# Kernel tuning notes

Hardware: AMD Instinct MI355X
Metric: run time of the kernel (lower is better)

The kernel has to match this reference:

```python
import jax, jax.numpy as jnp
import numpy as np

BLOCK_SIZE = 64  # weights per (scale, zero_point) block along in_features


def _dequant(q_weights, q_scales, q_zp):
    # q_weights: [N, K] int codes in [0,16); q_scales/q_zp: [N, K//BLOCK_SIZE]
    N, K = q_weights.shape
    nb = K // BLOCK_SIZE
    q = q_weights.reshape(N, nb, BLOCK_SIZE).astype(q_scales.dtype)
    zp = q_zp.reshape(N, nb, 1).astype(q_scales.dtype)
    s = q_scales.reshape(N, nb, 1)
    return ((q - zp) * s).reshape(N, K)  # [N, K] float


def setup_inputs() -> dict:
    key = jax.random.key(0)
    k1, k2, k3, k4, k5 = jax.random.split(key, 5)
    M, K, N = 4096, 4096, 11008
    nb = K // BLOCK_SIZE
    return {
        "input": jax.random.normal(k1, (M, K), dtype=jnp.float32),
        "q_weights": jax.random.randint(k2, (N, K), 0, 16, dtype=jnp.int32),
        "q_scales": jax.random.uniform(k3, (N, nb), dtype=jnp.float32, minval=0.01, maxval=0.05),
        "q_zp": jax.random.randint(k4, (N, nb), 0, 16, dtype=jnp.int32),
        "bias": jax.random.normal(k5, (N,), dtype=jnp.float32),
    }


def reference(input, q_weights, q_scales, q_zp, bias):
    # Blockwise int4 dequant + GEMM: out[m, n] = sum_k input[m, k] * w[n, k]
    w = _dequant(q_weights, q_scales, q_zp)          # [N, K]
    out = jnp.einsum("mk,nk->mn", input, w)          # [M, N]
    return out + bias[None, :]
```

## Files before the change

kernel.cpp:

```cpp
#include <hip/hip_runtime.h>


#define BM 128
#define BN 128
#define BK 64
#define LDSN 72

typedef __attribute__((ext_vector_type(8))) short bf16x8;
typedef __attribute__((ext_vector_type(4))) float f32x4;

__device__ __forceinline__ unsigned short f2bf(float f) {
    union { float f; unsigned int u; } v; v.f = f;
    unsigned int u = v.u;
    u += 0x7FFFu + ((u >> 16) & 1u);
    return (unsigned short)(u >> 16);
}
__device__ __forceinline__ unsigned int pack2(float a, float b) {
    return (unsigned int)f2bf(a) | ((unsigned int)f2bf(b) << 16);
}

__device__ __forceinline__ void gl_lds16(const void* gp, void* lp) {
    __builtin_amdgcn_global_load_lds(
        (const __attribute__((address_space(1))) unsigned int*)gp,
        (__attribute__((address_space(3))) unsigned int*)lp,
        16, 0, 0);
}

__global__ __launch_bounds__(256)
void a2bf_kernel(const float* __restrict__ A, unsigned short* __restrict__ Ab,
                 long total4)
{
    long t = (long)blockIdx.x * blockDim.x + threadIdx.x;
    if (t >= total4) return;
    float4 v = ((const float4*)A)[t];
    uint2 p; p.x = pack2(v.x, v.y); p.y = pack2(v.z, v.w);
    ((uint2*)Ab)[t] = p;
}

__global__ __launch_bounds__(256)
void dequant_kernel(const int* __restrict__ Q, const float* __restrict__ S,
                    const int* __restrict__ Zp, unsigned short* __restrict__ W,
                    int K, int nb)
{
    const int n = blockIdx.y;
    const int k = (blockIdx.x * 256 + threadIdx.x) * 8;
    if (k >= K) return;
    const int kb = k >> 6;
    const float s  = S[(size_t)n * nb + kb];
    const float zs = (float)Zp[(size_t)n * nb + kb] * s;
    const int4* qp = (const int4*)(Q + (size_t)n * K + k);
    int4 q0 = qp[0], q1 = qp[1];
    uint4 o;
    o.x = pack2((float)q0.x * s - zs, (float)q0.y * s - zs);
    o.y = pack2((float)q0.z * s - zs, (float)q0.w * s - zs);
    o.z = pack2((float)q1.x * s - zs, (float)q1.y * s - zs);
    o.w = pack2((float)q1.z * s - zs, (float)q1.w * s - zs);
    *(uint4*)(W + (size_t)n * K + k) = o;
}


#define G8_BARRIER() do { asm volatile("" ::: "memory");                    \
    __builtin_amdgcn_s_barrier(); asm volatile("" ::: "memory"); } while (0)
#define G8_VMCNT(n) asm volatile("s_waitcnt vmcnt(" #n ")" ::: "memory")
#define G8_LGKM0()  do { asm volatile("s_waitcnt lgkmcnt(0)" ::: "memory"); \
    __builtin_amdgcn_sched_barrier(0); } while (0)

#define G8_STAGE(G, kt, h, base, b)                                          \
  do {                                                                       \
    const unsigned short* _s = (G) + (long)(kt) * 64 + (long)(h) * 128 * K;  \
    gl_lds16(_s + aoff0, (base) + (b) * 32768 + (h) * 16384 + lds0);         \
    gl_lds16(_s + aoff1, (base) + (b) * 32768 + (h) * 16384 + lds1);         \
  } while (0)

#define G8_LOAD_AF(b, mh)                                                    \
  { _Pragma("unroll") for (int _i = 0; _i < 4; ++_i) {                       \
      const int _ra = (mh) * 128 + arow + _i * 16;                           \
      const char* _pa = AsB + (b) * 32768 + _ra * 128;                       \
      af[_i][0] = *(const bf16x8*)(_pa + ck0);                               \
      af[_i][1] = *(const bf16x8*)(_pa + ck1);                               \
  } }

#define G8_LOAD_BF(b, nh)                                                    \
  { _Pragma("unroll") for (int _j = 0; _j < 2; ++_j) {                       \
      const int _rb = (nh) * 128 + brow + _j * 16;                           \
      const char* _pb = BsB + (b) * 32768 + _rb * 128;                       \
      bfg[_j][0] = *(const bf16x8*)(_pb + ck0);                              \
      bfg[_j][1] = *(const bf16x8*)(_pb + ck1);                              \
  } }

#define G8_MFMA(q)                                                           \
  __builtin_amdgcn_s_setprio(1);                                             \
  { _Pragma("unroll") for (int _i = 0; _i < 4; ++_i)                         \
    _Pragma("unroll") for (int _j = 0; _j < 2; ++_j) {                       \
      acc[q][_i][_j] = __builtin_amdgcn_mfma_f32_16x16x32_bf16(              \
          af[_i][0], bfg[_j][0], acc[q][_i][_j], 0, 0, 0);                   \
      acc[q][_i][_j] = __builtin_amdgcn_mfma_f32_16x16x32_bf16(              \
          af[_i][1], bfg[_j][1], acc[q][_i][_j], 0, 0, 0);                   \
  } }                                                                        \
  __builtin_amdgcn_s_setprio(0);

__global__ __launch_bounds__(512, 2)
void gemm8_kernel(const unsigned short* __restrict__ Ab,
                  const unsigned short* __restrict__ Wb,
                  const float* __restrict__ bias, float* __restrict__ C,
                  int M, int N, int K)
{
    __shared__ __align__(16) unsigned short As[2][256][64];
    __shared__ __align__(16) unsigned short Bs[2][256][64];

    const int tid  = threadIdx.x;
    const int m0   = blockIdx.x * 256;
    const int n0   = blockIdx.y * 256;
    const int lane = tid & 63;
    const int wave = tid >> 6;
    const int ww   = wave >> 2;
    const int wv   = wave & 3;
    const int fr   = lane & 15;
    const int quad = lane >> 4;
    const int sw   = fr & 7;

    const int rl0 = tid >> 3;
    const int rl1 = (512 + tid) >> 3;
    const int pp  = tid & 7;
    const long aoff0 = (long)rl0 * K + (long)((pp ^ (rl0 & 7)) * 8);
    const long aoff1 = (long)rl1 * K + (long)((pp ^ (rl1 & 7)) * 8);
    const int lds0 = tid * 16;
    const int lds1 = (512 + tid) * 16;

    const int ck0 = (quad ^ sw) * 16;
    const int ck1 = ((4 + quad) ^ sw) * 16;
    const int arow = ww * 64 + fr;
    const int brow = wv * 32 + fr;

    char* AsB = (char*)&As[0][0][0];
    char* BsB = (char*)&Bs[0][0][0];

    const unsigned short* Ag = Ab + (size_t)m0 * K;
    const unsigned short* Bg = Wb + (size_t)n0 * K;

    f32x4 acc[4][4][2];
    #pragma unroll
    for (int q = 0; q < 4; ++q)
        #pragma unroll
        for (int i = 0; i < 4; ++i)
            #pragma unroll
            for (int j = 0; j < 2; ++j)
                acc[q][i][j] = (f32x4){0.f, 0.f, 0.f, 0.f};

    bf16x8 af[4][2], bfg[2][2];

    G8_STAGE(Ag, 0, 0, AsB, 0);
    G8_STAGE(Bg, 0, 0, BsB, 0);
    G8_STAGE(Ag, 0, 1, AsB, 0);
    G8_STAGE(Bg, 0, 1, BsB, 0);
    G8_STAGE(Ag, 1, 0, AsB, 1);
    G8_STAGE(Bg, 1, 0, BsB, 1);
    G8_VMCNT(4);
    G8_BARRIER();

    const int nit = K / 128;
    for (int it = 0; it < nit - 1; ++it) {
        const int t = 2 * it;
        G8_LOAD_AF(0, 0); G8_LOAD_BF(0, 0);
        G8_STAGE(Ag, t + 1, 1, AsB, 1);
        G8_BARRIER(); G8_LGKM0();
        G8_MFMA(0);
        G8_VMCNT(6);
        G8_BARRIER();
        G8_LOAD_BF(0, 1);
        G8_STAGE(Bg, t + 1, 1, BsB, 1);
        G8_BARRIER(); G8_LGKM0();
        G8_MFMA(1);
        G8_BARRIER();
        G8_LOAD_AF(0, 1); G8_LOAD_BF(0, 0);
        G8_STAGE(Ag, t + 2, 0, AsB, 0);
        G8_BARRIER(); G8_LGKM0();
        G8_MFMA(2);
        G8_BARRIER();
        G8_LOAD_BF(0, 1);
        G8_STAGE(Bg, t + 2, 0, BsB, 0);
        G8_BARRIER(); G8_LGKM0();
        G8_MFMA(3);
        G8_VMCNT(8);
        G8_BARRIER();
        G8_LOAD_AF(1, 0); G8_LOAD_BF(1, 0);
        G8_STAGE(Ag, t + 2, 1, AsB, 0);
        G8_BARRIER(); G8_LGKM0();
        G8_MFMA(0);
        G8_VMCNT(6);
        G8_BARRIER();
        G8_LOAD_BF(1, 1);
        G8_STAGE(Bg, t + 2, 1, BsB, 0);
        G8_BARRIER(); G8_LGKM0();
        G8_MFMA(1);
        G8_BARRIER();
        G8_LOAD_AF(1, 1); G8_LOAD_BF(1, 0);
        G8_STAGE(Ag, t + 3, 0, AsB, 1);
        G8_BARRIER(); G8_LGKM0();
        G8_MFMA(2);
        G8_BARRIER();
        G8_LOAD_BF(1, 1);
        G8_STAGE(Bg, t + 3, 0, BsB, 1);
        G8_BARRIER(); G8_LGKM0();
        G8_MFMA(3);
        G8_VMCNT(8);
        G8_BARRIER();
    }
    {
        const int t = 2 * (nit - 1);
        G8_LOAD_AF(0, 0); G8_LOAD_BF(0, 0);
        G8_STAGE(Ag, t + 1, 1, AsB, 1);
        G8_BARRIER(); G8_LGKM0(); G8_MFMA(0); G8_VMCNT(6); G8_BARRIER();

        G8_LOAD_BF(0, 1);
        G8_STAGE(Bg, t + 1, 1, BsB, 1);
        G8_BARRIER(); G8_LGKM0(); G8_MFMA(1); G8_BARRIER();

        G8_LOAD_AF(0, 1); G8_LOAD_BF(0, 0);
        G8_BARRIER(); G8_LGKM0(); G8_MFMA(2); G8_BARRIER();

        G8_LOAD_BF(0, 1);
        G8_BARRIER(); G8_LGKM0(); G8_MFMA(3); G8_VMCNT(4); G8_BARRIER();

        G8_LOAD_AF(1, 0); G8_LOAD_BF(1, 0);
        G8_BARRIER(); G8_LGKM0(); G8_MFMA(0); G8_VMCNT(0); G8_BARRIER();

        G8_LOAD_BF(1, 1);
        G8_BARRIER(); G8_LGKM0(); G8_MFMA(1); G8_BARRIER();

        G8_LOAD_AF(1, 1); G8_LOAD_BF(1, 0);
        G8_BARRIER(); G8_LGKM0(); G8_MFMA(2); G8_BARRIER();

        G8_LOAD_BF(1, 1);
        G8_BARRIER(); G8_LGKM0(); G8_MFMA(3); G8_BARRIER();
    }

    #pragma unroll
    for (int q = 0; q < 4; ++q) {
        const int mh = q >> 1, nh = q & 1;
        #pragma unroll
        for (int j = 0; j < 2; ++j) {
            const int n = n0 + nh * 128 + brow + j * 16;
            const float bv = bias[n];
            #pragma unroll
            for (int i = 0; i < 4; ++i) {
                const int mb = m0 + mh * 128 + ww * 64 + i * 16 + quad * 4;
                #pragma unroll
                for (int r = 0; r < 4; ++r)
                    C[(size_t)(mb + r) * N + n] = acc[q][i][j][r] + bv;
            }
        }
    }
}

__global__ __launch_bounds__(256, 2)
void gemm_bt_kernel(const unsigned short* __restrict__ Ab,
                    const unsigned short* __restrict__ Wb,
                    const float* __restrict__ bias, float* __restrict__ C,
                    int M, int N, int K)
{
    __shared__ __align__(16) unsigned short As[BM * BK];
    __shared__ __align__(16) unsigned short Bs[BN * BK];

    const int tid = threadIdx.x;
    const int m0  = blockIdx.x * BM;
    const int n0  = blockIdx.y * BN;

    const int lane = tid & 63;
    const int wave = tid >> 6;
    const int wm   = (wave >> 1) * 64;
    const int wn   = (wave & 1) * 64;
    const int fr   = lane & 15;
    const int quad = lane >> 4;
    const int sw   = fr & 7;

    f32x4 acc[4][4];
    #pragma unroll
    for (int i = 0; i < 4; ++i)
        #pragma unroll
        for (int j = 0; j < 4; ++j)
            acc[i][j] = (f32x4){0.f, 0.f, 0.f, 0.f};

    const int ktiles = K / BK;
    for (int kt = 0; kt < ktiles; ++kt) {
        const int k0 = kt * BK;
        #pragma unroll
        for (int i = 0; i < 4; ++i) {
            const int c    = i * 256 + tid;
            const int row  = c >> 3;
            const int g    = (c & 7) ^ (row & 7);
            const int cole = g * 8;
            gl_lds16(Ab + (size_t)(m0 + row) * K + k0 + cole, (char*)As + c * 16);
            gl_lds16(Wb + (size_t)(n0 + row) * K + k0 + cole, (char*)Bs + c * 16);
        }
        __syncthreads();

        #pragma unroll
        for (int ks = 0; ks < 2; ++ks) {
            bf16x8 af[4], bfg[4];
            #pragma unroll
            for (int i = 0; i < 4; ++i) {
                const int row = wm + i * 16 + fr;
                const int p   = (ks * 4 + quad) ^ sw;
                af[i] = *(const bf16x8*)&As[row * BK + p * 8];
            }
            #pragma unroll
            for (int j = 0; j < 4; ++j) {
                const int row = wn + j * 16 + fr;
                const int p   = (ks * 4 + quad) ^ sw;
                bfg[j] = *(const bf16x8*)&Bs[row * BK + p * 8];
            }
            #pragma unroll
            for (int i = 0; i < 4; ++i)
                #pragma unroll
                for (int j = 0; j < 4; ++j)
                    acc[i][j] = __builtin_amdgcn_mfma_f32_16x16x32_bf16(af[i], bfg[j], acc[i][j], 0, 0, 0);
        }
        __syncthreads();
    }

    #pragma unroll
    for (int j = 0; j < 4; ++j) {
        const int n = n0 + wn + j * 16 + fr;
        const float bv = bias[n];
        #pragma unroll
        for (int i = 0; i < 4; ++i) {
            const int mb = m0 + wm + i * 16 + quad * 4;
            #pragma unroll
            for (int r = 0; r < 4; ++r)
                C[(size_t)(mb + r) * N + n] = acc[i][j][r] + bv;
        }
    }
}

__global__ __launch_bounds__(256, 2)
void q4gemm_fused(const float* __restrict__ A, const int* __restrict__ Q,
                  const float* __restrict__ S, const int* __restrict__ Zp,
                  const float* __restrict__ bias, float* __restrict__ C,
                  int M, int N, int K, int nb)
{
    __shared__ __align__(16) unsigned short As[BM * LDSN];
    __shared__ __align__(16) unsigned short Bs[BN * LDSN];

    const int tid = threadIdx.x;
    const int m0  = blockIdx.x * BM;
    const int n0  = blockIdx.y * BN;
    const int srow = tid >> 4;
    const int scol = (tid & 15) << 2;
    const int lane = tid & 63;
    const int wave = tid >> 6;
    const int wm   = (wave >> 1) * 64;
    const int wn   = (wave & 1) * 64;
    const int fr   = lane & 15;
    const int quad = lane >> 4;

    f32x4 acc[4][4];
    #pragma unroll
    for (int i = 0; i < 4; ++i)
        #pragma unroll
        for (int j = 0; j < 4; ++j)
            acc[i][j] = (f32x4){0.f, 0.f, 0.f, 0.f};

    const int ktiles = K / BK;
    for (int kt = 0; kt < ktiles; ++kt) {
        const int k0 = kt * BK;
        #pragma unroll
        for (int i = 0; i < 8; ++i) {
            const int r = i * 16 + srow;
            const float4 v = *(const float4*)(A + (size_t)(m0 + r) * K + k0 + scol);
            uint2 p; p.x = pack2(v.x, v.y); p.y = pack2(v.z, v.w);
            *(uint2*)&As[r * LDSN + scol] = p;
        }
        #pragma unroll
        for (int i = 0; i < 8; ++i) {
            const int r = i * 16 + srow;
            const int n = n0 + r;
            const int4 q = *(const int4*)(Q + (size_t)n * K + k0 + scol);
            const float s  = S[(size_t)n * nb + kt];
            const float zs = (float)Zp[(size_t)n * nb + kt] * s;
            uint2 p;
            p.x = pack2((float)q.x * s - zs, (float)q.y * s - zs);
            p.y = pack2((float)q.z * s - zs, (float)q.w * s - zs);
            *(uint2*)&Bs[r * LDSN + scol] = p;
        }
        __syncthreads();
        #pragma unroll
        for (int ks = 0; ks < 2; ++ks) {
            bf16x8 af[4], bfg[4];
            #pragma unroll
            for (int i = 0; i < 4; ++i)
                af[i] = *(const bf16x8*)&As[(wm + i * 16 + fr) * LDSN + ks * 32 + quad * 8];
            #pragma unroll
            for (int j = 0; j < 4; ++j)
                bfg[j] = *(const bf16x8*)&Bs[(wn + j * 16 + fr) * LDSN + ks * 32 + quad * 8];
            #pragma unroll
            for (int i = 0; i < 4; ++i)
                #pragma unroll
                for (int j = 0; j < 4; ++j)
                    acc[i][j] = __builtin_amdgcn_mfma_f32_16x16x32_bf16(af[i], bfg[j], acc[i][j], 0, 0, 0);
        }
        __syncthreads();
    }
    #pragma unroll
    for (int j = 0; j < 4; ++j) {
        const int n = n0 + wn + j * 16 + fr;
        const float bv = bias[n];
        #pragma unroll
        for (int i = 0; i < 4; ++i) {
            const int mb = m0 + wm + i * 16 + quad * 4;
            #pragma unroll
            for (int r = 0; r < 4; ++r)
                C[(size_t)(mb + r) * N + n] = acc[i][j][r] + bv;
        }
    }
}

extern "C" void kernel_launch(void* const* d_in, const int* in_sizes, int n_in,
                              void* d_out, int out_size, void* d_ws, size_t ws_size,
                              hipStream_t stream) {
    const float* A    = (const float*)d_in[0];
    const int*   Q    = (const int*)d_in[1];
    const float* S    = (const float*)d_in[2];
    const int*   Zp   = (const int*)d_in[3];
    const float* bias = (const float*)d_in[4];
    float* C = (float*)d_out;

    const int N  = in_sizes[4];
    const int K  = in_sizes[1] / N;
    const int M  = in_sizes[0] / K;
    const int nb = in_sizes[2] / N;

    const size_t needA = (size_t)M * K * 2;
    const size_t needW = (size_t)N * K * 2;

    if (ws_size >= needA + needW) {
        unsigned short* Ab = (unsigned short*)d_ws;
        unsigned short* Wb = (unsigned short*)((char*)d_ws + needA);

        long total4 = (long)M * K / 4;
        a2bf_kernel<<<(unsigned)((total4 + 255) / 256), 256, 0, stream>>>(A, Ab, total4);

        dim3 dq_grid((K / 8 + 255) / 256, N);
        dequant_kernel<<<dq_grid, 256, 0, stream>>>(Q, S, Zp, Wb, K, nb);

        if ((M % 256) == 0 && (N % 256) == 0 && (K % 128) == 0 && K >= 256) {
            dim3 grid(M / 256, N / 256);
            gemm8_kernel<<<grid, dim3(512), 0, stream>>>(Ab, Wb, bias, C, M, N, K);
        } else {
            dim3 grid(M / BM, N / BN);
            gemm_bt_kernel<<<grid, dim3(256), 0, stream>>>(Ab, Wb, bias, C, M, N, K);
        }
    } else {
        dim3 grid(M / BM, N / BN);
        q4gemm_fused<<<grid, dim3(256), 0, stream>>>(A, Q, S, Zp, bias, C, M, N, K, nb);
    }
}
```

Before: 726.3 us.

## Fuse prep kernels, remap GEMM workgroups across XCDs, use immediate-offset LDS reads

Merges the activation bf16 conversion and weight dequant into one launch, which removes a kernel launch and its tail. Flattens the GEMM grid to 1D and remaps workgroup IDs in groups of 8, apparently so that tiles sharing operands run on the same XCD and reuse its L2. Replaces compiler-generated LDS fragment loads with inline-asm ds_read_b128 that use precomputed base addresses and immediate offsets, cutting address arithmetic, and simplifies the barrier macro to raw s_barrier. The fast path now also requires K to be a multiple of 2048.

```diff
diff --git a/kernel.cpp b/kernel.cpp
--- a/kernel.cpp
+++ b/kernel.cpp
@@ -26,43 +26,55 @@
         16, 0, 0);
 }
 
+__device__ __forceinline__ unsigned lds_off(const void* p) {
+    return (unsigned)(unsigned long long)
+        (const __attribute__((address_space(3))) void*)p;
+}
+
+template<int IMM>
+__device__ __forceinline__ bf16x8 ds128(unsigned a) {
+    bf16x8 d;
+    asm volatile("ds_read_b128 %0, %1 offset:%2"
+                 : "=v"(d) : "v"(a), "i"(IMM));
+    return d;
+}
+
 __global__ __launch_bounds__(256)
-void a2bf_kernel(const float* __restrict__ A, unsigned short* __restrict__ Ab,
-                 long total4)
+void prep_kernel(const float* __restrict__ A, const int* __restrict__ Q,
+                 const float* __restrict__ S, const int* __restrict__ Zp,
+                 unsigned short* __restrict__ Ab, unsigned short* __restrict__ W,
+                 int M, int K, int nb)
 {
-    long t = (long)blockIdx.x * blockDim.x + threadIdx.x;
-    if (t >= total4) return;
-    float4 v = ((const float4*)A)[t];
-    uint2 p; p.x = pack2(v.x, v.y); p.y = pack2(v.z, v.w);
-    ((uint2*)Ab)[t] = p;
-}
-
-__global__ __launch_bounds__(256)
-void dequant_kernel(const int* __restrict__ Q, const float* __restrict__ S,
-                    const int* __restrict__ Zp, unsigned short* __restrict__ W,
-                    int K, int nb)
-{
-    const int n = blockIdx.y;
+    const int y = blockIdx.y;
     const int k = (blockIdx.x * 256 + threadIdx.x) * 8;
     if (k >= K) return;
-    const int kb = k >> 6;
-    const float s  = S[(size_t)n * nb + kb];
-    const float zs = (float)Zp[(size_t)n * nb + kb] * s;
-    const int4* qp = (const int4*)(Q + (size_t)n * K + k);
-    int4 q0 = qp[0], q1 = qp[1];
-    uint4 o;
-    o.x = pack2((float)q0.x * s - zs, (float)q0.y * s - zs);
-    o.y = pack2((float)q0.z * s - zs, (float)q0.w * s - zs);
-    o.z = pack2((float)q1.x * s - zs, (float)q1.y * s - zs);
-    o.w = pack2((float)q1.z * s - zs, (float)q1.w * s - zs);
-    *(uint4*)(W + (size_t)n * K + k) = o;
-}
-
-
-#define G8_BARRIER() do { asm volatile("" ::: "memory");                    \
-    __builtin_amdgcn_s_barrier(); asm volatile("" ::: "memory"); } while (0)
-#define G8_VMCNT(n) asm volatile("s_waitcnt vmcnt(" #n ")" ::: "memory")
-#define G8_LGKM0()  do { asm volatile("s_waitcnt lgkmcnt(0)" ::: "memory"); \
+    if (y < M) {
+        const float4* ap = (const float4*)(A + (size_t)y * K + k);
+        float4 a0 = ap[0], a1 = ap[1];
+        uint4 o;
+        o.x = pack2(a0.x, a0.y); o.y = pack2(a0.z, a0.w);
+        o.z = pack2(a1.x, a1.y); o.w = pack2(a1.z, a1.w);
+        *(uint4*)(Ab + (size_t)y * K + k) = o;
+    } else {
+        const int n = y - M;
+        const int kb = k >> 6;
+        const float s  = S[(size_t)n * nb + kb];
+        const float zs = (float)Zp[(size_t)n * nb + kb] * s;
+        const int4* qp = (const int4*)(Q + (size_t)n * K + k);
+        int4 q0 = qp[0], q1 = qp[1];
+        uint4 o;
+        o.x = pack2((float)q0.x * s - zs, (float)q0.y * s - zs);
+        o.y = pack2((float)q0.z * s - zs, (float)q0.w * s - zs);
+        o.z = pack2((float)q1.x * s - zs, (float)q1.y * s - zs);
+        o.w = pack2((float)q1.z * s - zs, (float)q1.w * s - zs);
+        *(uint4*)(W + (size_t)n * K + k) = o;
+    }
+}
+
+
+#define G8_BARRIER() asm volatile("s_barrier" ::: "memory")
+#define G8_VMCNT(n)  asm volatile("s_waitcnt vmcnt(" #n ")" ::: "memory")
+#define G8_LGKM0()   do { asm volatile("s_waitcnt lgkmcnt(0)" ::: "memory"); \
     __builtin_amdgcn_sched_barrier(0); } while (0)
 
 #define G8_STAGE(G, kt, h, base, b)                                          \
@@ -73,20 +85,20 @@
   } while (0)
 
 #define G8_LOAD_AF(b, mh)                                                    \
-  { _Pragma("unroll") for (int _i = 0; _i < 4; ++_i) {                       \
-      const int _ra = (mh) * 128 + arow + _i * 16;                           \
-      const char* _pa = AsB + (b) * 32768 + _ra * 128;                       \
-      af[_i][0] = *(const bf16x8*)(_pa + ck0);                               \
-      af[_i][1] = *(const bf16x8*)(_pa + ck1);                               \
-  } }
+  af[0][0] = ds128<(b)*32768 + (mh)*16384 + 0*2048>(pA0);                    \
+  af[1][0] = ds128<(b)*32768 + (mh)*16384 + 1*2048>(pA0);                    \
+  af[2][0] = ds128<(b)*32768 + (mh)*16384 + 2*2048>(pA0);                    \
+  af[3][0] = ds128<(b)*32768 + (mh)*16384 + 3*2048>(pA0);                    \
+  af[0][1] = ds128<(b)*32768 + (mh)*16384 + 0*2048>(pA1);                    \
+  af[1][1] = ds128<(b)*32768 + (mh)*16384 + 1*2048>(pA1);                    \
+  af[2][1] = ds128<(b)*32768 + (mh)*16384 + 2*2048>(pA1);                    \
+  af[3][1] = ds128<(b)*32768 + (mh)*16384 + 3*2048>(pA1);
 
 #define G8_LOAD_BF(b, nh)                                                    \
-  { _Pragma("unroll") for (int _j = 0; _j < 2; ++_j) {                       \
-      const int _rb = (nh) * 128 + brow + _j * 16;                           \
-      const char* _pb = BsB + (b) * 32768 + _rb * 128;                       \
-      bfg[_j][0] = *(const bf16x8*)(_pb + ck0);                              \
-      bfg[_j][1] = *(const bf16x8*)(_pb + ck1);                              \
-  } }
+  bfg[0][0] = ds128<(b)*32768 + (nh)*16384 + 0*2048>(pB0);                   \
+  bfg[1][0] = ds128<(b)*32768 + (nh)*16384 + 1*2048>(pB0);                   \
+  bfg[0][1] = ds128<(b)*32768 + (nh)*16384 + 0*2048>(pB1);                   \
+  bfg[1][1] = ds128<(b)*32768 + (nh)*16384 + 1*2048>(pB1);
 
 #define G8_MFMA(q)                                                           \
   __builtin_amdgcn_s_setprio(1);                                             \
@@ -109,8 +121,17 @@
     __shared__ __align__(16) unsigned short Bs[2][256][64];
 
     const int tid  = threadIdx.x;
-    const int m0   = blockIdx.x * 256;
-    const int n0   = blockIdx.y * 256;
+
+    const int nwg = gridDim.x;
+    int wg = blockIdx.x;
+    {
+        const int q8 = nwg >> 3, r8 = nwg & 7, x = wg & 7, s = wg >> 3;
+        wg = (x < r8 ? x * (q8 + 1) : r8 * (q8 + 1) + (x - r8) * q8) + s;
+    }
+    const int gx = M / 256;
+    const int m0 = (wg % gx) * 256;
+    const int n0 = (wg / gx) * 256;
+
     const int lane = tid & 63;
     const int wave = tid >> 6;
     const int ww   = wave >> 2;
@@ -127,13 +148,17 @@
     const int lds0 = tid * 16;
     const int lds1 = (512 + tid) * 16;
 
-    const int ck0 = (quad ^ sw) * 16;
-    const int ck1 = ((4 + quad) ^ sw) * 16;
+    const int ck0 = ((quad    ) ^ sw) * 16;
+    const int ck1 = ((quad + 4) ^ sw) * 16;
     const int arow = ww * 64 + fr;
     const int brow = wv * 32 + fr;
 
     char* AsB = (char*)&As[0][0][0];
     char* BsB = (char*)&Bs[0][0][0];
+    const unsigned pA0 = lds_off(AsB) + arow * 128 + ck0;
+    const unsigned pA1 = lds_off(AsB) + arow * 128 + ck1;
+    const unsigned pB0 = lds_off(BsB) + brow * 128 + ck0;
+    const unsigned pB1 = lds_off(BsB) + brow * 128 + ck1;
 
     const unsigned short* Ag = Ab + (size_t)m0 * K;
     const unsigned short* Bg = Wb + (size_t)n0 * K;
@@ -161,45 +186,45 @@
     const int nit = K / 128;
     for (int it = 0; it < nit - 1; ++it) {
         const int t = 2 * it;
-        G8_LOAD_AF(0, 0); G8_LOAD_BF(0, 0);
+        G8_LOAD_AF(0, 0) G8_LOAD_BF(0, 0)
         G8_STAGE(Ag, t + 1, 1, AsB, 1);
         G8_BARRIER(); G8_LGKM0();
         G8_MFMA(0);
         G8_VMCNT(6);
         G8_BARRIER();
-        G8_LOAD_BF(0, 1);
+        G8_LOAD_BF(0, 1)
         G8_STAGE(Bg, t + 1, 1, BsB, 1);
         G8_BARRIER(); G8_LGKM0();
         G8_MFMA(1);
         G8_BARRIER();
-        G8_LOAD_AF(0, 1); G8_LOAD_BF(0, 0);
+        G8_LOAD_AF(0, 1) G8_LOAD_BF(0, 0)
         G8_STAGE(Ag, t + 2, 0, AsB, 0);
         G8_BARRIER(); G8_LGKM0();
         G8_MFMA(2);
         G8_BARRIER();
-        G8_LOAD_BF(0, 1);
+        G8_LOAD_BF(0, 1)
         G8_STAGE(Bg, t + 2, 0, BsB, 0);
         G8_BARRIER(); G8_LGKM0();
         G8_MFMA(3);
         G8_VMCNT(8);
         G8_BARRIER();
-        G8_LOAD_AF(1, 0); G8_LOAD_BF(1, 0);
+        G8_LOAD_AF(1, 0) G8_LOAD_BF(1, 0)
         G8_STAGE(Ag, t + 2, 1, AsB, 0);
         G8_BARRIER(); G8_LGKM0();
         G8_MFMA(0);
         G8_VMCNT(6);
         G8_BARRIER();
-        G8_LOAD_BF(1, 1);
+        G8_LOAD_BF(1, 1)
         G8_STAGE(Bg, t + 2, 1, BsB, 0);
         G8_BARRIER(); G8_LGKM0();
         G8_MFMA(1);
         G8_BARRIER();
-        G8_LOAD_AF(1, 1); G8_LOAD_BF(1, 0);
+        G8_LOAD_AF(1, 1) G8_LOAD_BF(1, 0)
         G8_STAGE(Ag, t + 3, 0, AsB, 1);
         G8_BARRIER(); G8_LGKM0();
         G8_MFMA(2);
         G8_BARRIER();
-        G8_LOAD_BF(1, 1);
+        G8_LOAD_BF(1, 1)
         G8_STAGE(Bg, t + 3, 0, BsB, 1);
         G8_BARRIER(); G8_LGKM0();
         G8_MFMA(3);
@@ -208,30 +233,30 @@
     }
     {
         const int t = 2 * (nit - 1);
-        G8_LOAD_AF(0, 0); G8_LOAD_BF(0, 0);
+        G8_LOAD_AF(0, 0) G8_LOAD_BF(0, 0)
         G8_STAGE(Ag, t + 1, 1, AsB, 1);
         G8_BARRIER(); G8_LGKM0(); G8_MFMA(0); G8_VMCNT(6); G8_BARRIER();
 
-        G8_LOAD_BF(0, 1);
+        G8_LOAD_BF(0, 1)
         G8_STAGE(Bg, t + 1, 1, BsB, 1);
         G8_BARRIER(); G8_LGKM0(); G8_MFMA(1); G8_BARRIER();
 
-        G8_LOAD_AF(0, 1); G8_LOAD_BF(0, 0);
+        G8_LOAD_AF(0, 1) G8_LOAD_BF(0, 0)
         G8_BARRIER(); G8_LGKM0(); G8_MFMA(2); G8_BARRIER();
 
-        G8_LOAD_BF(0, 1);
+        G8_LOAD_BF(0, 1)
         G8_BARRIER(); G8_LGKM0(); G8_MFMA(3); G8_VMCNT(4); G8_BARRIER();
 
-        G8_LOAD_AF(1, 0); G8_LOAD_BF(1, 0);
+        G8_LOAD_AF(1, 0) G8_LOAD_BF(1, 0)
         G8_BARRIER(); G8_LGKM0(); G8_MFMA(0); G8_VMCNT(0); G8_BARRIER();
 
-        G8_LOAD_BF(1, 1);
+        G8_LOAD_BF(1, 1)
         G8_BARRIER(); G8_LGKM0(); G8_MFMA(1); G8_BARRIER();
 
-        G8_LOAD_AF(1, 1); G8_LOAD_BF(1, 0);
+        G8_LOAD_AF(1, 1) G8_LOAD_BF(1, 0)
         G8_BARRIER(); G8_LGKM0(); G8_MFMA(2); G8_BARRIER();
 
-        G8_LOAD_BF(1, 1);
+        G8_LOAD_BF(1, 1)
         G8_BARRIER(); G8_LGKM0(); G8_MFMA(3); G8_BARRIER();
     }
 
@@ -433,19 +458,16 @@
     const size_t needA = (size_t)M * K * 2;
     const size_t needW = (size_t)N * K * 2;
 
-    if (ws_size >= needA + needW) {
+    if (ws_size >= needA + needW && (K % 2048) == 0) {
         unsigned short* Ab = (unsigned short*)d_ws;
         unsigned short* Wb = (unsigned short*)((char*)d_ws + needA);
 
-        long total4 = (long)M * K / 4;
-        a2bf_kernel<<<(unsigned)((total4 + 255) / 256), 256, 0, stream>>>(A, Ab, total4);
-
-        dim3 dq_grid((K / 8 + 255) / 256, N);
-        dequant_kernel<<<dq_grid, 256, 0, stream>>>(Q, S, Zp, Wb, K, nb);
+        dim3 pgrid(K / 2048, M + N);
+        prep_kernel<<<pgrid, 256, 0, stream>>>(A, Q, S, Zp, Ab, Wb, M, K, nb);
 
         if ((M % 256) == 0 && (N % 256) == 0 && (K % 128) == 0 && K >= 256) {
-            dim3 grid(M / 256, N / 256);
-            gemm8_kernel<<<grid, dim3(512), 0, stream>>>(Ab, Wb, bias, C, M, N, K);
+            gemm8_kernel<<<dim3((M / 256) * (N / 256)), dim3(512), 0, stream>>>(
+                Ab, Wb, bias, C, M, N, K);
         } else {
             dim3 grid(M / BM, N / BN);
             gemm_bt_kernel<<<grid, dim3(256), 0, stream>>>(Ab, Wb, bias, C, M, N, K);
```

New measurement: 658.5 us. -9.3%, faster.
